# Kernel tuning notes

Hardware: AMD Instinct MI355X
Metric: run time of the kernel (lower is better)

The kernel has to match this reference:

```python
import jax, jax.numpy as jnp
import numpy as np

B, S, G, F = 8, 4096, 128, 32


def setup_inputs() -> dict:
    key = jax.random.key(0)
    k1, k2 = jax.random.split(key)
    x = jax.random.normal(k1, (B, S, F), dtype=jnp.float32)
    centers = jax.random.uniform(k2, (G, F), dtype=jnp.float32)  # torch.rand init
    covariance = jnp.tile(jnp.eye(F, dtype=jnp.float32), (G, 1, 1))  # eye repeated per gaussian
    return {"x": x, "centers": centers, "covariance": covariance}


def reference(x, centers, covariance):
    # x: [B,S,F], centers: [G,F], covariance: [G,F,F] -> out [B,S,G]
    feature_dim = centers.shape[1]
    diff = x[:, :, None, :] - centers[None, None, :, :]          # [B,S,G,F]
    cov_inv = jnp.linalg.inv(covariance)                          # [G,F,F]
    det_cov = jnp.linalg.det(covariance)                          # [G]
    # batched Mahalanobis distance per gaussian
    mahalanobis = jnp.einsum('bsgi,gij,bsgj->bsg', diff, cov_inv, diff)
    normalization = jnp.log((2 * jnp.pi) ** feature_dim * det_cov)  # [G]
    log_probs = -0.5 * (mahalanobis + normalization[None, None, :])
    return jnp.exp(log_probs)
```

## Files before the change

### kernel.cpp

```cpp
#include <hip/hip_runtime.h>
#include <math.h>


#define GG 128
#define FF 32
#define NPTS (8 * 4096)
#define NIDB 16


__device__ __forceinline__ int load_eflag(const int* __restrict__ eflagArr) {
  int ef = 0;
  #pragma unroll
  for (int i = 0; i < NIDB; ++i) ef |= eflagArr[i];
  return ef;
}

__global__ __launch_bounds__(256) void gm_pre_ident(
    const float* __restrict__ centers, const float* __restrict__ cov,
    float* __restrict__ wbuf, float* __restrict__ beta,
    int* __restrict__ eflagArr)
{
  const int b = blockIdx.x;
  const int t = threadIdx.x;
  const float4* cv = (const float4*)(cov + (size_t)b * 8 * 1024);
  bool bad = false;
  #pragma unroll
  for (int i = 0; i < 8; ++i) {
    const int idx = t + i * 256;
    const float4 v = cv[idx];
    const int rc = (idx * 4) & 1023;
    const int r = rc >> 5, c0 = rc & 31;
    bad |= (v.x != ((c0     == r) ? 1.f : 0.f));
    bad |= (v.y != ((c0 + 1 == r) ? 1.f : 0.f));
    bad |= (v.z != ((c0 + 2 == r) ? 1.f : 0.f));
    bad |= (v.w != ((c0 + 3 == r) ? 1.f : 0.f));
  }
  __shared__ int sbad[4];
  const unsigned long long bal = __ballot(bad);
  if ((t & 63) == 0) sbad[t >> 6] = (bal != 0ULL) ? 1 : 0;
  __syncthreads();
  const int anybad = sbad[0] | sbad[1] | sbad[2] | sbad[3];
  if (t == 0) eflagArr[b] = anybad;
  if (anybad) return;

  if (t < 64) {
    const float4* cc = (const float4*)(centers + (size_t)b * 8 * 32);
    const float4 u = cc[t];
    ((float4*)(wbuf + (size_t)b * 8 * 32))[t] = u;
    float s = fmaf(u.x, u.x, fmaf(u.y, u.y, fmaf(u.z, u.z, u.w * u.w)));
    s += __shfl_xor(s, 1);
    s += __shfl_xor(s, 2);
    s += __shfl_xor(s, 4);
    if ((t & 7) == 0) beta[b * 8 + (t >> 3)] = s + 58.8120661251f;
  }
}

__global__ __launch_bounds__(64) void gm_pre_general(
    const float* __restrict__ centers, const float* __restrict__ cov,
    float* __restrict__ wbuf, float* __restrict__ beta,
    float* __restrict__ Ebuf, const int* __restrict__ eflagArr)
{
  if (!load_eflag(eflagArr)) return;
  const int g = blockIdx.x;
  const int t = threadIdx.x;
  const int r = t & 31;

  float row[64];
  {
    const float4* src = (const float4*)(cov + (size_t)g * 1024 + r * 32);
    #pragma unroll
    for (int i = 0; i < 8; ++i) {
      float4 v = src[i];
      row[i*4+0] = v.x; row[i*4+1] = v.y; row[i*4+2] = v.z; row[i*4+3] = v.w;
    }
    #pragma unroll
    for (int c = 0; c < 32; ++c) row[32 + c] = (c == r) ? 1.f : 0.f;
  }

  float logdet = 0.f;
  float dsign = 1.f;

  #pragma unroll
  for (int p = 0; p < 32; ++p) {
    float av = (t >= p && t < 32) ? fabsf(row[p]) : -1.f;
    int ridx = (t < 32) ? t : 63;
    #pragma unroll
    for (int off = 32; off > 0; off >>= 1) {
      float ov = __shfl_xor(av, off);
      int   oi = __shfl_xor(ridx, off);
      if (ov > av || (ov == av && oi < ridx)) { av = ov; ridx = oi; }
    }
    const int pr = ridx;
    if (pr != p) {
      const int srcl = (r == p) ? pr : ((r == pr) ? p : r);
      #pragma unroll
      for (int c = p; c < 64; ++c) row[c] = __shfl(row[c], srcl);
      dsign = -dsign;
    }
    float piv = __shfl(row[p], p);
    logdet += logf(fabsf(piv));
    if (piv < 0.f) dsign = -dsign;
    const float rp = 1.f / piv;
    if (r == p) {
      #pragma unroll
      for (int c = p; c < 64; ++c) row[c] *= rp;
    }
    const float fac = (r == p) ? 0.f : row[p];
    #pragma unroll
    for (int c = p; c < 64; ++c) {
      float prc = __shfl(row[c], p);
      row[c] = fmaf(-fac, prc, row[c]);
    }
  }

  const float* cg = centers + (size_t)g * 32;
  float w = 0.f;
  #pragma unroll
  for (int j = 0; j < 32; ++j) w = fmaf(row[32 + j], cg[j], w);
  if (t < 32) wbuf[(size_t)g * 32 + r] = w;

  float val = (t < 32) ? w * cg[r] : 0.f;
  #pragma unroll
  for (int off = 32; off > 0; off >>= 1) val += __shfl_xor(val, off);
  if (t == 0) {
    float norm = 58.8120661251f + logdet;
    if (dsign < 0.f) norm = __builtin_nanf("");
    beta[g] = val + norm;
  }

  if (t < 32) {
    float4* Eg = (float4*)(Ebuf + (size_t)g * 1024 + r * 32);
    #pragma unroll
    for (int i = 0; i < 8; ++i) {
      float4 e;
      e.x = row[32 + i*4 + 0] - ((i*4 + 0 == r) ? 1.f : 0.f);
      e.y = row[32 + i*4 + 1] - ((i*4 + 1 == r) ? 1.f : 0.f);
      e.z = row[32 + i*4 + 2] - ((i*4 + 2 == r) ? 1.f : 0.f);
      e.w = row[32 + i*4 + 3] - ((i*4 + 3 == r) ? 1.f : 0.f);
      Eg[i] = e;
    }
  }
}

__global__ __launch_bounds__(256) void gm_fast(
    const float* __restrict__ x, const float* __restrict__ wbuf,
    const float* __restrict__ beta, const int* __restrict__ eflagArr,
    float* __restrict__ out)
{
  if (load_eflag(eflagArr)) return;
  const int t = threadIdx.x;
  const int lane = t & 63;
  const int wv = t >> 6;
  const int g0 = lane * 2;

  float4 w01[16];
  {
    const float4* ws = (const float4*)(wbuf + (size_t)g0 * 32);
    #pragma unroll
    for (int i = 0; i < 16; ++i) w01[i] = ws[i];
  }
  const float b0 = beta[g0];
  const float b1 = beta[g0 + 1];

  const int p0 = blockIdx.x * 64 + wv * 16;
  #pragma unroll 4
  for (int pi = 0; pi < 16; ++pi) {
    const int p = p0 + pi;
    const float4* xp = (const float4*)(x + (size_t)p * 32);
    float a0 = 0.f, a1 = 0.f, a2 = 0.f, a3 = 0.f;
    float c0 = 0.f, c1 = 0.f, c2 = 0.f, c3 = 0.f;
    float n0 = 0.f, n1 = 0.f, n2 = 0.f, n3 = 0.f;
    #pragma unroll
    for (int i = 0; i < 8; ++i) {
      const float4 v = xp[i];
      a0 = fmaf(w01[i].x, v.x, a0);     a1 = fmaf(w01[i].y, v.y, a1);
      a2 = fmaf(w01[i].z, v.z, a2);     a3 = fmaf(w01[i].w, v.w, a3);
      c0 = fmaf(w01[8+i].x, v.x, c0);   c1 = fmaf(w01[8+i].y, v.y, c1);
      c2 = fmaf(w01[8+i].z, v.z, c2);   c3 = fmaf(w01[8+i].w, v.w, c3);
      n0 = fmaf(v.x, v.x, n0);          n1 = fmaf(v.y, v.y, n1);
      n2 = fmaf(v.z, v.z, n2);          n3 = fmaf(v.w, v.w, n3);
    }
    const float dA = (a0 + a1) + (a2 + a3);
    const float dB = (c0 + c1) + (c2 + c3);
    const float nn = (n0 + n1) + (n2 + n3);
    const float m0 = nn - 2.f * dA + b0;
    const float m1 = nn - 2.f * dB + b1;
    float2 o;
    o.x = __expf(-0.5f * m0);
    o.y = __expf(-0.5f * m1);
    *(float2*)(out + (size_t)p * 128 + g0) = o;
  }
}

__global__ __launch_bounds__(256) void gm_general(
    const float* __restrict__ x, const float* __restrict__ wbuf,
    const float* __restrict__ beta, const float* __restrict__ Ebuf,
    const int* __restrict__ eflagArr, float* __restrict__ out)
{
  if (!load_eflag(eflagArr)) return;
  __shared__ float xs[32 * 32];
  __shared__ float xnorm[32];
  const int t = threadIdx.x;
  const int g = t & 127;
  const int ph = t >> 7;
  const int pbase = blockIdx.x * 32;

  ((float4*)xs)[t] = ((const float4*)(x + (size_t)pbase * 32))[t];

  float wr[32];
  {
    const float4* wsrc = (const float4*)(wbuf + (size_t)g * 32);
    #pragma unroll
    for (int i = 0; i < 8; ++i) {
      float4 v = wsrc[i];
      wr[i*4+0] = v.x; wr[i*4+1] = v.y; wr[i*4+2] = v.z; wr[i*4+3] = v.w;
    }
  }
  const float betag = beta[g];
  __syncthreads();

  if (t < 32) {
    float s = 0.f;
    const float4* xp = (const float4*)(xs + t * 32);
    #pragma unroll
    for (int i = 0; i < 8; ++i) {
      float4 v = xp[i];
      s = fmaf(v.x, v.x, fmaf(v.y, v.y, fmaf(v.z, v.z, fmaf(v.w, v.w, s))));
    }
    xnorm[t] = s;
  }
  __syncthreads();

  for (int p = ph; p < 32; p += 2) {
    float xv[32];
    const float4* xp = (const float4*)(xs + p * 32);
    #pragma unroll
    for (int i = 0; i < 8; ++i) {
      float4 v = xp[i];
      xv[i*4+0] = v.x; xv[i*4+1] = v.y; xv[i*4+2] = v.z; xv[i*4+3] = v.w;
    }
    float dot = 0.f;
    #pragma unroll
    for (int k = 0; k < 32; ++k) dot = fmaf(wr[k], xv[k], dot);
    float quad = 0.f;
    const float* Eg = Ebuf + (size_t)g * 1024;
    for (int i = 0; i < 32; ++i) {
      float exi = 0.f;
      const float4* er = (const float4*)(Eg + i * 32);
      #pragma unroll
      for (int j = 0; j < 8; ++j) {
        float4 e = er[j];
        exi = fmaf(e.x, xv[j*4+0],
              fmaf(e.y, xv[j*4+1],
              fmaf(e.z, xv[j*4+2],
              fmaf(e.w, xv[j*4+3], exi))));
      }
      quad = fmaf(xv[i], exi, quad);
    }
    float m = xnorm[p] + quad - 2.f * dot + betag;
    out[(size_t)(pbase + p) * 128 + g] = __expf(-0.5f * m);
  }
}

extern "C" void kernel_launch(void* const* d_in, const int* in_sizes, int n_in,
                              void* d_out, int out_size, void* d_ws, size_t ws_size,
                              hipStream_t stream) {
  const float* x       = (const float*)d_in[0];
  const float* centers = (const float*)d_in[1];
  const float* cov     = (const float*)d_in[2];
  float* out = (float*)d_out;

  char* ws = (char*)d_ws;
  int*   eflagArr = (int*)ws;
  float* beta  = (float*)(ws + 256);
  float* wbuf  = (float*)(ws + 1024);
  float* Ebuf  = (float*)(ws + 32768);

  hipLaunchKernelGGL(gm_pre_ident, dim3(NIDB), dim3(256), 0, stream,
                     centers, cov, wbuf, beta, eflagArr);
  hipLaunchKernelGGL(gm_pre_general, dim3(GG), dim3(64), 0, stream,
                     centers, cov, wbuf, beta, Ebuf, eflagArr);
  hipLaunchKernelGGL(gm_fast, dim3(NPTS / 64), dim3(256), 0, stream,
                     x, wbuf, beta, eflagArr, out);
  hipLaunchKernelGGL(gm_general, dim3(NPTS / 32), dim3(256), 0, stream,
                     x, wbuf, beta, Ebuf, eflagArr, out);
}
```

Before: 84.01 us.

## Merge preprocessing and main kernels to cut launches from four to two

The two preprocessing kernels become one per-gaussian kernel that checks whether the covariance is the identity, writes per-gaussian flags, and writes zero correction matrices for identity covariances. The fast and general main kernels become one kernel that branches on the combined flag, and the fast path reads centers directly and computes the squared norms itself. The intent is to remove two kernel launches and the early-exit blocks of the unused path. In exchange, each main block now reads 128 flags, and the general path works on 64 points per block.

```diff
diff --git a/kernel.cpp b/kernel.cpp
--- a/kernel.cpp
+++ b/kernel.cpp
@@ -5,66 +5,63 @@
 #define GG 128
 #define FF 32
 #define NPTS (8 * 4096)
-#define NIDB 16
+#define LOG_NORM_CONST 58.8120661251f
 
 
 __device__ __forceinline__ int load_eflag(const int* __restrict__ eflagArr) {
   int ef = 0;
-  #pragma unroll
-  for (int i = 0; i < NIDB; ++i) ef |= eflagArr[i];
+  const int4* ea = (const int4*)eflagArr;
+  #pragma unroll
+  for (int i = 0; i < 32; ++i) {
+    int4 v = ea[i];
+    ef |= v.x | v.y | v.z | v.w;
+  }
   return ef;
 }
 
-__global__ __launch_bounds__(256) void gm_pre_ident(
+__global__ __launch_bounds__(64) void gm_pre(
     const float* __restrict__ centers, const float* __restrict__ cov,
     float* __restrict__ wbuf, float* __restrict__ beta,
-    int* __restrict__ eflagArr)
+    float* __restrict__ Ebuf, int* __restrict__ eflagArr)
 {
-  const int b = blockIdx.x;
+  const int g = blockIdx.x;
   const int t = threadIdx.x;
-  const float4* cv = (const float4*)(cov + (size_t)b * 8 * 1024);
+
+  const float4* cv = (const float4*)(cov + (size_t)g * 1024);
   bool bad = false;
   #pragma unroll
-  for (int i = 0; i < 8; ++i) {
-    const int idx = t + i * 256;
+  for (int i = 0; i < 4; ++i) {
+    const int idx = t + i * 64;
     const float4 v = cv[idx];
-    const int rc = (idx * 4) & 1023;
-    const int r = rc >> 5, c0 = rc & 31;
+    const int e = idx * 4;
+    const int r = e >> 5, c0 = e & 31;
     bad |= (v.x != ((c0     == r) ? 1.f : 0.f));
     bad |= (v.y != ((c0 + 1 == r) ? 1.f : 0.f));
     bad |= (v.z != ((c0 + 2 == r) ? 1.f : 0.f));
     bad |= (v.w != ((c0 + 3 == r) ? 1.f : 0.f));
   }
-  __shared__ int sbad[4];
   const unsigned long long bal = __ballot(bad);
-  if ((t & 63) == 0) sbad[t >> 6] = (bal != 0ULL) ? 1 : 0;
-  __syncthreads();
-  const int anybad = sbad[0] | sbad[1] | sbad[2] | sbad[3];
-  if (t == 0) eflagArr[b] = anybad;
-  if (anybad) return;
-
-  if (t < 64) {
-    const float4* cc = (const float4*)(centers + (size_t)b * 8 * 32);
-    const float4 u = cc[t];
-    ((float4*)(wbuf + (size_t)b * 8 * 32))[t] = u;
-    float s = fmaf(u.x, u.x, fmaf(u.y, u.y, fmaf(u.z, u.z, u.w * u.w)));
-    s += __shfl_xor(s, 1);
-    s += __shfl_xor(s, 2);
-    s += __shfl_xor(s, 4);
-    if ((t & 7) == 0) beta[b * 8 + (t >> 3)] = s + 58.8120661251f;
-  }
-}
-
-__global__ __launch_bounds__(64) void gm_pre_general(
-    const float* __restrict__ centers, const float* __restrict__ cov,
-    float* __restrict__ wbuf, float* __restrict__ beta,
-    float* __restrict__ Ebuf, const int* __restrict__ eflagArr)
-{
-  if (!load_eflag(eflagArr)) return;
-  const int g = blockIdx.x;
-  const int t = threadIdx.x;
+  if (t == 0) eflagArr[g] = (bal != 0ULL) ? 1 : 0;
+
+  if (bal == 0ULL) {
+    const float4* cc = (const float4*)(centers + (size_t)g * 32);
+    if (t < 8) {
+      const float4 u = cc[t];
+      ((float4*)(wbuf + (size_t)g * 32))[t] = u;
+      float s = fmaf(u.x, u.x, fmaf(u.y, u.y, fmaf(u.z, u.z, u.w * u.w)));
+      s += __shfl_xor(s, 1);
+      s += __shfl_xor(s, 2);
+      s += __shfl_xor(s, 4);
+      if (t == 0) beta[g] = s + LOG_NORM_CONST;
+    }
+    float4 z; z.x = z.y = z.z = z.w = 0.f;
+    float4* Eg = (float4*)(Ebuf + (size_t)g * 1024);
+    #pragma unroll
+    for (int i = 0; i < 4; ++i) Eg[t + i * 64] = z;
+    return;
+  }
+
   const int r = t & 31;
-
   float row[64];
   {
     const float4* src = (const float4*)(cov + (size_t)g * 1024 + r * 32);
@@ -123,7 +120,7 @@
   #pragma unroll
   for (int off = 32; off > 0; off >>= 1) val += __shfl_xor(val, off);
   if (t == 0) {
-    float norm = 58.8120661251f + logdet;
+    float norm = LOG_NORM_CONST + logdet;
     if (dsign < 0.f) norm = __builtin_nanf("");
     beta[g] = val + norm;
   }
@@ -142,70 +139,77 @@
   }
 }
 
-__global__ __launch_bounds__(256) void gm_fast(
-    const float* __restrict__ x, const float* __restrict__ wbuf,
-    const float* __restrict__ beta, const int* __restrict__ eflagArr,
+__global__ __launch_bounds__(256) void gm_main(
+    const float* __restrict__ x, const float* __restrict__ centers,
+    const float* __restrict__ wbuf, const float* __restrict__ beta,
+    const float* __restrict__ Ebuf, const int* __restrict__ eflagArr,
     float* __restrict__ out)
 {
-  if (load_eflag(eflagArr)) return;
   const int t = threadIdx.x;
-  const int lane = t & 63;
-  const int wv = t >> 6;
-  const int g0 = lane * 2;
-
-  float4 w01[16];
-  {
-    const float4* ws = (const float4*)(wbuf + (size_t)g0 * 32);
-    #pragma unroll
-    for (int i = 0; i < 16; ++i) w01[i] = ws[i];
-  }
-  const float b0 = beta[g0];
-  const float b1 = beta[g0 + 1];
-
-  const int p0 = blockIdx.x * 64 + wv * 16;
-  #pragma unroll 4
-  for (int pi = 0; pi < 16; ++pi) {
-    const int p = p0 + pi;
-    const float4* xp = (const float4*)(x + (size_t)p * 32);
-    float a0 = 0.f, a1 = 0.f, a2 = 0.f, a3 = 0.f;
-    float c0 = 0.f, c1 = 0.f, c2 = 0.f, c3 = 0.f;
-    float n0 = 0.f, n1 = 0.f, n2 = 0.f, n3 = 0.f;
-    #pragma unroll
-    for (int i = 0; i < 8; ++i) {
-      const float4 v = xp[i];
-      a0 = fmaf(w01[i].x, v.x, a0);     a1 = fmaf(w01[i].y, v.y, a1);
-      a2 = fmaf(w01[i].z, v.z, a2);     a3 = fmaf(w01[i].w, v.w, a3);
-      c0 = fmaf(w01[8+i].x, v.x, c0);   c1 = fmaf(w01[8+i].y, v.y, c1);
-      c2 = fmaf(w01[8+i].z, v.z, c2);   c3 = fmaf(w01[8+i].w, v.w, c3);
-      n0 = fmaf(v.x, v.x, n0);          n1 = fmaf(v.y, v.y, n1);
-      n2 = fmaf(v.z, v.z, n2);          n3 = fmaf(v.w, v.w, n3);
-    }
-    const float dA = (a0 + a1) + (a2 + a3);
-    const float dB = (c0 + c1) + (c2 + c3);
-    const float nn = (n0 + n1) + (n2 + n3);
-    const float m0 = nn - 2.f * dA + b0;
-    const float m1 = nn - 2.f * dB + b1;
-    float2 o;
-    o.x = __expf(-0.5f * m0);
-    o.y = __expf(-0.5f * m1);
-    *(float2*)(out + (size_t)p * 128 + g0) = o;
-  }
-}
-
-__global__ __launch_bounds__(256) void gm_general(
-    const float* __restrict__ x, const float* __restrict__ wbuf,
-    const float* __restrict__ beta, const float* __restrict__ Ebuf,
-    const int* __restrict__ eflagArr, float* __restrict__ out)
-{
-  if (!load_eflag(eflagArr)) return;
-  __shared__ float xs[32 * 32];
-  __shared__ float xnorm[32];
-  const int t = threadIdx.x;
+  const int ef = load_eflag(eflagArr);
+
+  if (!ef) {
+    const int lane = t & 63;
+    const int wv = t >> 6;
+    const int g0 = lane * 2;
+
+    float4 c01[16];
+    {
+      const float4* cs = (const float4*)(centers + (size_t)g0 * 32);
+      #pragma unroll
+      for (int i = 0; i < 16; ++i) c01[i] = cs[i];
+    }
+    float s0 = 0.f, s1 = 0.f;
+    #pragma unroll
+    for (int i = 0; i < 8; ++i) {
+      const float4 a = c01[i], b = c01[8 + i];
+      s0 = fmaf(a.x, a.x, fmaf(a.y, a.y, fmaf(a.z, a.z, fmaf(a.w, a.w, s0))));
+      s1 = fmaf(b.x, b.x, fmaf(b.y, b.y, fmaf(b.z, b.z, fmaf(b.w, b.w, s1))));
+    }
+    const float b0 = s0 + LOG_NORM_CONST;
+    const float b1 = s1 + LOG_NORM_CONST;
+
+    const int p0 = blockIdx.x * 64 + wv * 16;
+    #pragma unroll 4
+    for (int pi = 0; pi < 16; ++pi) {
+      const int p = p0 + pi;
+      const float4* xp = (const float4*)(x + (size_t)p * 32);
+      float a0 = 0.f, a1 = 0.f, a2 = 0.f, a3 = 0.f;
+      float c0 = 0.f, c1 = 0.f, c2 = 0.f, c3 = 0.f;
+      float n0 = 0.f, n1 = 0.f, n2 = 0.f, n3 = 0.f;
+      #pragma unroll
+      for (int i = 0; i < 8; ++i) {
+        const float4 v = xp[i];
+        a0 = fmaf(c01[i].x, v.x, a0);     a1 = fmaf(c01[i].y, v.y, a1);
+        a2 = fmaf(c01[i].z, v.z, a2);     a3 = fmaf(c01[i].w, v.w, a3);
+        c0 = fmaf(c01[8+i].x, v.x, c0);   c1 = fmaf(c01[8+i].y, v.y, c1);
+        c2 = fmaf(c01[8+i].z, v.z, c2);   c3 = fmaf(c01[8+i].w, v.w, c3);
+        n0 = fmaf(v.x, v.x, n0);          n1 = fmaf(v.y, v.y, n1);
+        n2 = fmaf(v.z, v.z, n2);          n3 = fmaf(v.w, v.w, n3);
+      }
+      const float dA = (a0 + a1) + (a2 + a3);
+      const float dB = (c0 + c1) + (c2 + c3);
+      const float nn = (n0 + n1) + (n2 + n3);
+      float2 o;
+      o.x = __expf(-0.5f * (nn - 2.f * dA + b0));
+      o.y = __expf(-0.5f * (nn - 2.f * dB + b1));
+      *(float2*)(out + (size_t)p * 128 + g0) = o;
+    }
+    return;
+  }
+
+  __shared__ float xs[64 * 32];
+  __shared__ float xnorm[64];
   const int g = t & 127;
   const int ph = t >> 7;
-  const int pbase = blockIdx.x * 32;
-
-  ((float4*)xs)[t] = ((const float4*)(x + (size_t)pbase * 32))[t];
+  const int pbase = blockIdx.x * 64;
+
+  {
+    const float4* xsrc = (const float4*)(x + (size_t)pbase * 32);
+    float4* xd = (float4*)xs;
+    xd[t] = xsrc[t];
+    xd[t + 256] = xsrc[t + 256];
+  }
 
   float wr[32];
   {
@@ -219,7 +223,7 @@
   const float betag = beta[g];
   __syncthreads();
 
-  if (t < 32) {
+  if (t < 64) {
     float s = 0.f;
     const float4* xp = (const float4*)(xs + t * 32);
     #pragma unroll
@@ -231,7 +235,7 @@
   }
   __syncthreads();
 
-  for (int p = ph; p < 32; p += 2) {
+  for (int p = ph; p < 64; p += 2) {
     float xv[32];
     const float4* xp = (const float4*)(xs + p * 32);
     #pragma unroll
@@ -272,16 +276,12 @@
 
   char* ws = (char*)d_ws;
   int*   eflagArr = (int*)ws;
-  float* beta  = (float*)(ws + 256);
-  float* wbuf  = (float*)(ws + 1024);
+  float* beta  = (float*)(ws + 1024);
+  float* wbuf  = (float*)(ws + 2048);
   float* Ebuf  = (float*)(ws + 32768);
 
-  hipLaunchKernelGGL(gm_pre_ident, dim3(NIDB), dim3(256), 0, stream,
-                     centers, cov, wbuf, beta, eflagArr);
-  hipLaunchKernelGGL(gm_pre_general, dim3(GG), dim3(64), 0, stream,
+  hipLaunchKernelGGL(gm_pre, dim3(GG), dim3(64), 0, stream,
                      centers, cov, wbuf, beta, Ebuf, eflagArr);
-  hipLaunchKernelGGL(gm_fast, dim3(NPTS / 64), dim3(256), 0, stream,
-                     x, wbuf, beta, eflagArr, out);
-  hipLaunchKernelGGL(gm_general, dim3(NPTS / 32), dim3(256), 0, stream,
-                     x, wbuf, beta, Ebuf, eflagArr, out);
-}
+  hipLaunchKernelGGL(gm_main, dim3(NPTS / 64), dim3(256), 0, stream,
+                     x, centers, wbuf, beta, Ebuf, eflagArr, out);
+}
```

After: 82.14 us. 2.2% less time.
